# Kernel tuning notes

Measured on AMD Instinct MI355X. Metric: run time of the kernel, lower is better.

## Reference

```python
import jax, jax.numpy as jnp
import numpy as np

B, C, H, W = 8, 256, 64, 64
CI = 128  # inter_channels
EPS = 1e-5

def conv1x1(x, w, b):
    # x:[B,C,H,W], w:[O,C], b:[O] -> [B,O,H,W]
    return jnp.einsum('bchw,oc->bohw', x, w) + b[None, :, None, None]

def maxpool2(t):
    b, c, h, w = t.shape
    return t.reshape(b, c, h // 2, 2, w // 2, 2).max(axis=(3, 5))

def setup_inputs() -> dict:
    key = jax.random.key(0)
    ks = jax.random.split(key, 11)
    s_in = 1.0 / np.sqrt(C)
    s_ci = 1.0 / np.sqrt(CI)
    return {
        'x':        jax.random.normal(ks[0], (B, C, H, W), jnp.float32),
        'g_w':      jax.random.normal(ks[1], (CI, C), jnp.float32) * s_in,
        'g_b':      jax.random.normal(ks[2], (CI,), jnp.float32) * s_in,
        'theta_w':  jax.random.normal(ks[3], (CI, C), jnp.float32) * s_in,
        'theta_b':  jax.random.normal(ks[4], (CI,), jnp.float32) * s_in,
        'phi_w':    jax.random.normal(ks[5], (CI, C), jnp.float32) * s_in,
        'phi_b':    jax.random.normal(ks[6], (CI,), jnp.float32) * s_in,
        'w_w':      jax.random.normal(ks[7], (C, CI), jnp.float32) * s_ci,
        'w_b':      jax.random.normal(ks[8], (C,), jnp.float32) * s_ci,
        'bn_gamma': jax.random.normal(ks[9], (C,), jnp.float32) * 0.1 + 1.0,
        'bn_beta':  jax.random.normal(ks[10], (C,), jnp.float32) * 0.1,
    }

def reference(x, g_w, g_b, theta_w, theta_b, phi_w, phi_b, w_w, w_b, bn_gamma, bn_beta):
    b, c, h, w = x.shape
    n = h * w
    # g and phi are sub-sampled with 2x2 max pool -> Ns = n // 4
    g_x = maxpool2(conv1x1(x, g_w, g_b)).reshape(b, CI, -1)      # [B,CI,Ns]
    g_x = g_x.transpose(0, 2, 1)                                  # [B,Ns,CI]
    theta_x = conv1x1(x, theta_w, theta_b).reshape(b, CI, n)
    theta_x = theta_x.transpose(0, 2, 1)                          # [B,N,CI]
    phi_x = maxpool2(conv1x1(x, phi_w, phi_b)).reshape(b, CI, -1)  # [B,CI,Ns]
    f = jnp.einsum('bnc,bcm->bnm', theta_x, phi_x)                # [B,N,Ns] (no 1/sqrt(d) scale, faithful)
    f_div_c = jax.nn.softmax(f, axis=-1)
    y = jnp.einsum('bnm,bmc->bnc', f_div_c, g_x)                  # [B,N,CI]
    y = y.transpose(0, 2, 1).reshape(b, CI, h, w)
    wy = conv1x1(y, w_w, w_b)                                     # [B,C,H,W]
    # BatchNorm2d in training mode: batch stats over (B,H,W)
    mean = wy.mean(axis=(0, 2, 3), keepdims=True)
    var = wy.var(axis=(0, 2, 3), keepdims=True)
    wy_bn = (wy - mean) * jax.lax.rsqrt(var + EPS)
    wy_bn = wy_bn * bn_gamma[None, :, None, None] + bn_beta[None, :, None, None]
    return wy_bn + x
```

## Files before the change

kernel.cpp:

```cpp
#include <hip/hip_runtime.h>
#include <hip/hip_bf16.h>
#include <hip/hip_fp16.h>
#include <math.h>

#define B 8
#define C 256
#define HH 64
#define WW 64
#define NN 4096
#define CI 128
#define NS 1024
#define EPS 1e-5f

typedef __attribute__((ext_vector_type(8))) _Float16 f16x8;
typedef __attribute__((ext_vector_type(4))) float f32x4;

static __device__ __forceinline__ unsigned short f2h_bits(float f) {
    return __half_as_ushort(__float2half(f));
}

__global__ __launch_bounds__(256) void k_prep(const float* __restrict__ tw,
        const float* __restrict__ pw, const float* __restrict__ gw,
        const float* __restrict__ ww, unsigned short* __restrict__ wh) {
    int idx = blockIdx.x * 256 + threadIdx.x;
    int sel = idx >> 15, off = idx & 32767;
    const float* src = (sel == 0) ? tw : (sel == 1) ? pw : (sel == 2) ? gw : ww;
    wh[idx] = f2h_bits(src[off]);
}

__global__ __launch_bounds__(256) void k_xt(const float* __restrict__ x,
                                            unsigned short* __restrict__ xh) {
    __shared__ float s_t[64 * 65];
    int n0 = blockIdx.x * 64;
    int c0 = blockIdx.y * 64;
    int b  = blockIdx.z;
    int tid = threadIdx.x;
    #pragma unroll
    for (int k = 0; k < 16; ++k) {
        int idx = tid + k * 256;
        int cl = idx >> 6, nl = idx & 63;
        s_t[cl * 65 + nl] = x[((size_t)b * C + c0 + cl) * NN + n0 + nl];
    }
    __syncthreads();
    #pragma unroll
    for (int k = 0; k < 8; ++k) {
        int idx = tid + k * 256;
        int nl = idx >> 5, cp = (idx & 31) * 2;
        ushort2 o;
        o.x = f2h_bits(s_t[cp * 65 + nl]);
        o.y = f2h_bits(s_t[(cp + 1) * 65 + nl]);
        *(ushort2*)&xh[((size_t)b * NN + n0 + nl) * C + c0 + cp] = o;
    }
}

__global__ __launch_bounds__(256) void k_conv_theta(const unsigned short* __restrict__ xh,
        const unsigned short* __restrict__ twh, const float* __restrict__ tb,
        unsigned short* __restrict__ theta) {
    int blk = blockIdx.x;
    int tid = threadIdx.x;
    int lane = tid & 63, wv = tid >> 6;
    int lr = lane & 15, lh = lane >> 4;
    int rowf = blk * 64 + wv * 16 + lr;

    f32x4 acc[8];
    #pragma unroll
    for (int i = 0; i < 8; ++i) acc[i] = (f32x4){0.f, 0.f, 0.f, 0.f};

    const unsigned short* ap = xh + (size_t)rowf * C + lh * 8;
    #pragma unroll
    for (int kc = 0; kc < 8; ++kc) {
        f16x8 a = *(const f16x8*)(ap + kc * 32);
        #pragma unroll
        for (int ct = 0; ct < 8; ++ct) {
            f16x8 bf = *(const f16x8*)&twh[(ct * 16 + lr) * C + kc * 32 + lh * 8];
            acc[ct] = __builtin_amdgcn_mfma_f32_16x16x32_f16(a, bf, acc[ct], 0, 0, 0);
        }
    }
    int rowo = blk * 64 + wv * 16 + lh * 4;
    #pragma unroll
    for (int ct = 0; ct < 8; ++ct) {
        int ci = ct * 16 + lr;
        float bias = tb[ci];
        #pragma unroll
        for (int r = 0; r < 4; ++r)
            theta[(size_t)(rowo + r) * CI + ci] = f2h_bits(acc[ct][r] + bias);
    }
}

__global__ __launch_bounds__(512) void k_conv_pool2(const unsigned short* __restrict__ xh,
        const unsigned short* __restrict__ pwh, const unsigned short* __restrict__ gwh,
        const float* __restrict__ pb, const float* __restrict__ gb_,
        unsigned short* __restrict__ phi, unsigned short* __restrict__ gout) {
    int blk = blockIdx.x;
    int b   = blk >> 5;
    int mh  = blk & 31;
    int tid = threadIdx.x;
    int lane = tid & 63, wv = tid >> 6;
    int lr = lane & 15, lh = lane >> 4;
    int wn = wv & 3, wc = wv >> 2;
    size_t row0 = (size_t)blk * 128;

    f32x4 aP0[4], aP1[4], aG0[4], aG1[4];
    #pragma unroll
    for (int i = 0; i < 4; ++i) {
        aP0[i] = (f32x4){0,0,0,0}; aP1[i] = (f32x4){0,0,0,0};
        aG0[i] = (f32x4){0,0,0,0}; aG1[i] = (f32x4){0,0,0,0};
    }

    const unsigned short* ap0 = xh + (row0 + wn * 16 + lr) * C + lh * 8;
    const unsigned short* ap1 = ap0 + (size_t)64 * C;
    #pragma unroll
    for (int kc = 0; kc < 8; ++kc) {
        f16x8 a0 = *(const f16x8*)(ap0 + kc * 32);
        f16x8 a1 = *(const f16x8*)(ap1 + kc * 32);
        #pragma unroll
        for (int ct = 0; ct < 4; ++ct) {
            int wrow = (wc * 64 + ct * 16 + lr) * C + kc * 32 + lh * 8;
            f16x8 bp = *(const f16x8*)&pwh[wrow];
            f16x8 bg = *(const f16x8*)&gwh[wrow];
            aP0[ct] = __builtin_amdgcn_mfma_f32_16x16x32_f16(a0, bp, aP0[ct], 0, 0, 0);
            aP1[ct] = __builtin_amdgcn_mfma_f32_16x16x32_f16(a1, bp, aP1[ct], 0, 0, 0);
            aG0[ct] = __builtin_amdgcn_mfma_f32_16x16x32_f16(a0, bg, aG0[ct], 0, 0, 0);
            aG1[ct] = __builtin_amdgcn_mfma_f32_16x16x32_f16(a1, bg, aG1[ct], 0, 0, 0);
        }
    }
    #pragma unroll
    for (int ct = 0; ct < 4; ++ct) {
        int ci = wc * 64 + ct * 16 + lr;
        float biasP = pb[ci], biasG = gb_[ci];
        #pragma unroll
        for (int j = 0; j < 2; ++j) {
            int m = mh * 32 + wn * 8 + lh * 2 + j;
            float vP = fmaxf(fmaxf(aP0[ct][2*j], aP0[ct][2*j+1]),
                             fmaxf(aP1[ct][2*j], aP1[ct][2*j+1])) + biasP;
            float vG = fmaxf(fmaxf(aG0[ct][2*j], aG0[ct][2*j+1]),
                             fmaxf(aG1[ct][2*j], aG1[ct][2*j+1])) + biasG;
            phi[((size_t)b * NS + m) * CI + ci]  = f2h_bits(vP);
            gout[((size_t)b * CI + ci) * NS + m] = f2h_bits(vG);
        }
    }
}

#define SPH 136
#define SG  72
#define SP  72
__global__ __launch_bounds__(256) void k_attn_mfma(const unsigned short* __restrict__ theta,
        const unsigned short* __restrict__ phi, const unsigned short* __restrict__ g,
        unsigned short* __restrict__ y) {
    __shared__ unsigned short s_ph[64 * SPH];
    __shared__ unsigned short s_g[128 * SG];
    __shared__ unsigned short s_p[64 * SP];
    int rb = blockIdx.x;
    int b  = blockIdx.y;
    int tid = threadIdx.x;
    int lane = tid & 63, wv = tid >> 6;
    int lr = lane & 15, lh = lane >> 4;
    int row0 = rb * 64;
    int wrow = wv * 16;

    f16x8 a_th[4];
    {
        const unsigned short* tp = theta + ((size_t)b * NN + row0 + wrow + lr) * CI + lh * 8;
        #pragma unroll
        for (int kc = 0; kc < 4; ++kc) a_th[kc] = *(const f16x8*)(tp + kc * 32);
    }

    f32x4 yacc[8];
    #pragma unroll
    for (int i = 0; i < 8; ++i) yacc[i] = (f32x4){0.f, 0.f, 0.f, 0.f};
    float mrun[4] = {-1e30f, -1e30f, -1e30f, -1e30f};
    float lrun[4] = {0.f, 0.f, 0.f, 0.f};

    for (int mt = 0; mt < 16; ++mt) {
        __syncthreads();
        {
            const ushort4* src = (const ushort4*)(phi + ((size_t)b * NS + mt * 64) * CI);
            #pragma unroll
            for (int k = 0; k < 8; ++k) {
                int t = tid + k * 256;
                int r = t >> 5, cq = t & 31;
                ushort4 vv = src[r * 32 + cq];
                *(ushort4*)&s_ph[r * SPH + cq * 4] = vv;
            }
            const ushort4* sg = (const ushort4*)(g + (size_t)b * CI * NS);
            #pragma unroll
            for (int k = 0; k < 8; ++k) {
                int t = tid + k * 256;
                int ci = t >> 4, cq = t & 15;
                ushort4 vv = sg[ci * 256 + mt * 16 + cq];
                *(ushort4*)&s_g[ci * SG + cq * 4] = vv;
            }
        }
        __syncthreads();

        f32x4 S[4];
        #pragma unroll
        for (int nt = 0; nt < 4; ++nt) S[nt] = (f32x4){0.f, 0.f, 0.f, 0.f};
        #pragma unroll
        for (int nt = 0; nt < 4; ++nt) {
            #pragma unroll
            for (int kc = 0; kc < 4; ++kc) {
                f16x8 bf = *(const f16x8*)&s_ph[(nt * 16 + lr) * SPH + kc * 32 + lh * 8];
                S[nt] = __builtin_amdgcn_mfma_f32_16x16x32_f16(a_th[kc], bf, S[nt], 0, 0, 0);
            }
        }

        float rmax[4], rs[4], scale[4];
        #pragma unroll
        for (int r = 0; r < 4; ++r)
            rmax[r] = fmaxf(fmaxf(S[0][r], S[1][r]), fmaxf(S[2][r], S[3][r]));
        #pragma unroll
        for (int s = 1; s < 16; s <<= 1) {
            #pragma unroll
            for (int r = 0; r < 4; ++r) rmax[r] = fmaxf(rmax[r], __shfl_xor(rmax[r], s));
        }
        #pragma unroll
        for (int r = 0; r < 4; ++r) {
            float mnew = fmaxf(mrun[r], rmax[r]);
            scale[r] = __expf(mrun[r] - mnew);
            mrun[r] = mnew;
            rs[r] = 0.f;
        }
        #pragma unroll
        for (int nt = 0; nt < 4; ++nt) {
            #pragma unroll
            for (int r = 0; r < 4; ++r) {
                float e = __expf(S[nt][r] - mrun[r]);
                S[nt][r] = e;
                rs[r] += e;
            }
        }
        #pragma unroll
        for (int s = 1; s < 16; s <<= 1) {
            #pragma unroll
            for (int r = 0; r < 4; ++r) rs[r] += __shfl_xor(rs[r], s);
        }
        #pragma unroll
        for (int r = 0; r < 4; ++r) lrun[r] = lrun[r] * scale[r] + rs[r];
        #pragma unroll
        for (int i = 0; i < 8; ++i) {
            #pragma unroll
            for (int r = 0; r < 4; ++r) yacc[i][r] *= scale[r];
        }
        #pragma unroll
        for (int nt = 0; nt < 4; ++nt) {
            #pragma unroll
            for (int r = 0; r < 4; ++r)
                s_p[(wrow + lh * 4 + r) * SP + nt * 16 + lr] = f2h_bits(S[nt][r]);
        }

        f16x8 a_p[2];
        #pragma unroll
        for (int kc = 0; kc < 2; ++kc)
            a_p[kc] = *(const f16x8*)&s_p[(wrow + lr) * SP + kc * 32 + lh * 8];
        #pragma unroll
        for (int ct = 0; ct < 8; ++ct) {
            #pragma unroll
            for (int kc = 0; kc < 2; ++kc) {
                f16x8 bg = *(const f16x8*)&s_g[(ct * 16 + lr) * SG + kc * 32 + lh * 8];
                yacc[ct] = __builtin_amdgcn_mfma_f32_16x16x32_f16(a_p[kc], bg, yacc[ct], 0, 0, 0);
            }
        }
    }

    float inv[4];
    #pragma unroll
    for (int r = 0; r < 4; ++r) inv[r] = 1.f / lrun[r];
    #pragma unroll
    for (int ct = 0; ct < 8; ++ct) {
        #pragma unroll
        for (int r = 0; r < 4; ++r)
            y[((size_t)b * NN + row0 + wrow + lh * 4 + r) * CI + ct * 16 + lr] =
                f2h_bits(yacc[ct][r] * inv[r]);
    }
}

__global__ __launch_bounds__(256) void k_wconv(const unsigned short* __restrict__ y,
        const unsigned short* __restrict__ wwh, const float* __restrict__ wb,
        float* __restrict__ wy) {
    int blk = blockIdx.x;
    int b   = blk >> 6;
    int nloc = (blk & 63) * 64;
    int tid = threadIdx.x;
    int lane = tid & 63, wv = tid >> 6;
    int lr = lane & 15, lh = lane >> 4;

    f32x4 acc[4][4];
    #pragma unroll
    for (int i = 0; i < 4; ++i)
        #pragma unroll
        for (int j = 0; j < 4; ++j) acc[i][j] = (f32x4){0.f, 0.f, 0.f, 0.f};

    const unsigned short* yb = y + ((size_t)b * NN + nloc) * CI;
    #pragma unroll
    for (int kc = 0; kc < 4; ++kc) {
        f16x8 a[4], bf[4];
        #pragma unroll
        for (int at = 0; at < 4; ++at)
            a[at] = *(const f16x8*)&wwh[(wv * 64 + at * 16 + lr) * CI + kc * 32 + lh * 8];
        #pragma unroll
        for (int bt = 0; bt < 4; ++bt)
            bf[bt] = *(const f16x8*)&yb[(size_t)(bt * 16 + lr) * CI + kc * 32 + lh * 8];
        #pragma unroll
        for (int at = 0; at < 4; ++at)
            #pragma unroll
            for (int bt = 0; bt < 4; ++bt)
                acc[at][bt] = __builtin_amdgcn_mfma_f32_16x16x32_f16(a[at], bf[bt], acc[at][bt], 0, 0, 0);
    }
    #pragma unroll
    for (int at = 0; at < 4; ++at) {
        #pragma unroll
        for (int r = 0; r < 4; ++r) {
            int co = wv * 64 + at * 16 + lh * 4 + r;
            float bias = wb[co];
            float* wp = wy + ((size_t)b * C + co) * NN + nloc;
            #pragma unroll
            for (int bt = 0; bt < 4; ++bt)
                wp[bt * 16 + lr] = acc[at][bt][r] + bias;
        }
    }
}

__global__ __launch_bounds__(256) void k_stats(const float* __restrict__ wy,
                                               float* __restrict__ stats) {
    int c = blockIdx.x;
    int tid = threadIdx.x;
    float s = 0.f, sq = 0.f;
    for (int b = 0; b < B; ++b) {
        const float* p = wy + ((size_t)b * C + c) * NN;
        #pragma unroll 4
        for (int k = 0; k < 16; ++k) {
            float v = p[tid + k * 256];
            s += v;
            sq = fmaf(v, v, sq);
        }
    }
    #pragma unroll
    for (int o = 32; o >= 1; o >>= 1) {
        s  += __shfl_down(s, o);
        sq += __shfl_down(sq, o);
    }
    __shared__ float rs[4], rq[4];
    int lane = tid & 63, wv = tid >> 6;
    if (lane == 0) { rs[wv] = s; rq[wv] = sq; }
    __syncthreads();
    if (tid == 0) {
        stats[c]       = rs[0] + rs[1] + rs[2] + rs[3];
        stats[256 + c] = rq[0] + rq[1] + rq[2] + rq[3];
    }
}

__global__ __launch_bounds__(256) void k_bn_out(const float* __restrict__ wy,
        const float* __restrict__ x, const float* __restrict__ stats,
        const float* __restrict__ gamma, const float* __restrict__ beta,
        float* __restrict__ out) {
    size_t idx = (size_t)blockIdx.x * 256 + threadIdx.x;
    int c = (int)(((idx * 4) >> 12) & 255);
    float mean = stats[c] * (1.f / 32768.f);
    float var  = stats[256 + c] * (1.f / 32768.f) - mean * mean;
    float sc = gamma[c] * rsqrtf(var + EPS);
    float sh = beta[c] - mean * sc;
    float4 w4 = ((const float4*)wy)[idx];
    float4 x4 = ((const float4*)x)[idx];
    float4 o;
    o.x = fmaf(w4.x, sc, sh) + x4.x;
    o.y = fmaf(w4.y, sc, sh) + x4.y;
    o.z = fmaf(w4.z, sc, sh) + x4.z;
    o.w = fmaf(w4.w, sc, sh) + x4.w;
    ((float4*)out)[idx] = o;
}

extern "C" void kernel_launch(void* const* d_in, const int* in_sizes, int n_in,
                              void* d_out, int out_size, void* d_ws, size_t ws_size,
                              hipStream_t stream) {
    const float* x    = (const float*)d_in[0];
    const float* g_w  = (const float*)d_in[1];
    const float* g_b  = (const float*)d_in[2];
    const float* th_w = (const float*)d_in[3];
    const float* th_b = (const float*)d_in[4];
    const float* ph_w = (const float*)d_in[5];
    const float* ph_b = (const float*)d_in[6];
    const float* w_w  = (const float*)d_in[7];
    const float* w_b  = (const float*)d_in[8];
    const float* bn_g = (const float*)d_in[9];
    const float* bn_b = (const float*)d_in[10];
    float* out = (float*)d_out;

    char* w0 = (char*)d_ws;
    float*          wy    = (float*)w0;
    unsigned short* xh    = (unsigned short*)w0;
    unsigned short* theta = (unsigned short*)(w0 + 16777216);
    unsigned short* wh    = (unsigned short*)(w0 + 33554432);
    unsigned short* twh   = wh;
    unsigned short* pwh   = wh + 32768;
    unsigned short* gwh   = wh + 65536;
    unsigned short* wwh   = wh + 98304;
    unsigned short* phi   = (unsigned short*)(w0 + 33816576);
    unsigned short* gx    = (unsigned short*)(w0 + 35913728);
    unsigned short* yh    = (unsigned short*)(w0 + 38010880);
    float*          stats = (float*)(w0 + 46399488);

    k_prep<<<512, 256, 0, stream>>>(th_w, ph_w, g_w, w_w, wh);
    k_xt<<<dim3(64, 4, B), 256, 0, stream>>>(x, xh);
    k_conv_theta<<<512, 256, 0, stream>>>(xh, twh, th_b, theta);
    k_conv_pool2<<<256, 512, 0, stream>>>(xh, pwh, gwh, ph_b, g_b, phi, gx);
    k_attn_mfma<<<dim3(64, B), 256, 0, stream>>>(theta, phi, gx, yh);
    k_wconv<<<512, 256, 0, stream>>>(yh, wwh, w_b, wy);
    k_stats<<<256, 256, 0, stream>>>(wy, stats);
    k_bn_out<<<8192, 256, 0, stream>>>(wy, x, stats, bn_g, bn_b, out);
}
```

Before: 150.2 us.

## Fuse conv kernels, double-buffer attention tiles, store wy in fp16 with fused stats

Weight conversion is folded into the transpose kernel, and the theta conv is merged into the phi/g pooling conv so each x tile is read once. The attention loop now prefetches the next phi/g tile into registers and double-buffers shared memory, using setprio around MFMA blocks. The w-conv writes wy as fp16 and emits per-block partial sums, which replaces the full-tensor stats pass with a small reduction and halves traffic in the BN kernel. Storing wy in fp16 loses precision before the batch norm.

```diff
diff --git a/kernel.cpp b/kernel.cpp
--- a/kernel.cpp
+++ b/kernel.cpp
@@ -18,23 +18,32 @@
 static __device__ __forceinline__ unsigned short f2h_bits(float f) {
     return __half_as_ushort(__float2half(f));
 }
-
-__global__ __launch_bounds__(256) void k_prep(const float* __restrict__ tw,
-        const float* __restrict__ pw, const float* __restrict__ gw,
-        const float* __restrict__ ww, unsigned short* __restrict__ wh) {
-    int idx = blockIdx.x * 256 + threadIdx.x;
-    int sel = idx >> 15, off = idx & 32767;
-    const float* src = (sel == 0) ? tw : (sel == 1) ? pw : (sel == 2) ? gw : ww;
-    wh[idx] = f2h_bits(src[off]);
+static __device__ __forceinline__ float h2f(unsigned short u) {
+    return __half2float(__ushort_as_half(u));
 }
 
 __global__ __launch_bounds__(256) void k_xt(const float* __restrict__ x,
-                                            unsigned short* __restrict__ xh) {
+        unsigned short* __restrict__ xh,
+        const float* __restrict__ tw, const float* __restrict__ pw,
+        const float* __restrict__ gw, const float* __restrict__ ww,
+        unsigned short* __restrict__ wh) {
+    int tid = threadIdx.x;
+    if (blockIdx.x == 64) {
+        int inst = blockIdx.y * B + blockIdx.z;
+        int base = inst * 4096;
+        #pragma unroll
+        for (int k = 0; k < 16; ++k) {
+            int idx = base + tid + k * 256;
+            int sel = idx >> 15, off = idx & 32767;
+            const float* src = (sel == 0) ? tw : (sel == 1) ? pw : (sel == 2) ? gw : ww;
+            wh[idx] = f2h_bits(src[off]);
+        }
+        return;
+    }
     __shared__ float s_t[64 * 65];
     int n0 = blockIdx.x * 64;
     int c0 = blockIdx.y * 64;
     int b  = blockIdx.z;
-    int tid = threadIdx.x;
     #pragma unroll
     for (int k = 0; k < 16; ++k) {
         int idx = tid + k * 256;
@@ -53,44 +62,12 @@
     }
 }
 
-__global__ __launch_bounds__(256) void k_conv_theta(const unsigned short* __restrict__ xh,
-        const unsigned short* __restrict__ twh, const float* __restrict__ tb,
-        unsigned short* __restrict__ theta) {
-    int blk = blockIdx.x;
-    int tid = threadIdx.x;
-    int lane = tid & 63, wv = tid >> 6;
-    int lr = lane & 15, lh = lane >> 4;
-    int rowf = blk * 64 + wv * 16 + lr;
-
-    f32x4 acc[8];
-    #pragma unroll
-    for (int i = 0; i < 8; ++i) acc[i] = (f32x4){0.f, 0.f, 0.f, 0.f};
-
-    const unsigned short* ap = xh + (size_t)rowf * C + lh * 8;
-    #pragma unroll
-    for (int kc = 0; kc < 8; ++kc) {
-        f16x8 a = *(const f16x8*)(ap + kc * 32);
-        #pragma unroll
-        for (int ct = 0; ct < 8; ++ct) {
-            f16x8 bf = *(const f16x8*)&twh[(ct * 16 + lr) * C + kc * 32 + lh * 8];
-            acc[ct] = __builtin_amdgcn_mfma_f32_16x16x32_f16(a, bf, acc[ct], 0, 0, 0);
-        }
-    }
-    int rowo = blk * 64 + wv * 16 + lh * 4;
-    #pragma unroll
-    for (int ct = 0; ct < 8; ++ct) {
-        int ci = ct * 16 + lr;
-        float bias = tb[ci];
-        #pragma unroll
-        for (int r = 0; r < 4; ++r)
-            theta[(size_t)(rowo + r) * CI + ci] = f2h_bits(acc[ct][r] + bias);
-    }
-}
-
-__global__ __launch_bounds__(512) void k_conv_pool2(const unsigned short* __restrict__ xh,
-        const unsigned short* __restrict__ pwh, const unsigned short* __restrict__ gwh,
-        const float* __restrict__ pb, const float* __restrict__ gb_,
-        unsigned short* __restrict__ phi, unsigned short* __restrict__ gout) {
+__global__ __launch_bounds__(512) void k_convs(const unsigned short* __restrict__ xh,
+        const unsigned short* __restrict__ twh, const unsigned short* __restrict__ pwh,
+        const unsigned short* __restrict__ gwh,
+        const float* __restrict__ tb, const float* __restrict__ pb, const float* __restrict__ gb_,
+        unsigned short* __restrict__ theta, unsigned short* __restrict__ phi,
+        unsigned short* __restrict__ gout) {
     int blk = blockIdx.x;
     int b   = blk >> 5;
     int mh  = blk & 31;
@@ -100,7 +77,10 @@
     int wn = wv & 3, wc = wv >> 2;
     size_t row0 = (size_t)blk * 128;
 
+    f32x4 accT[8];
     f32x4 aP0[4], aP1[4], aG0[4], aG1[4];
+    #pragma unroll
+    for (int i = 0; i < 8; ++i) accT[i] = (f32x4){0,0,0,0};
     #pragma unroll
     for (int i = 0; i < 4; ++i) {
         aP0[i] = (f32x4){0,0,0,0}; aP1[i] = (f32x4){0,0,0,0};
@@ -113,6 +93,12 @@
     for (int kc = 0; kc < 8; ++kc) {
         f16x8 a0 = *(const f16x8*)(ap0 + kc * 32);
         f16x8 a1 = *(const f16x8*)(ap1 + kc * 32);
+        f16x8 aT = (wv < 4) ? a0 : a1;
+        #pragma unroll
+        for (int ct = 0; ct < 8; ++ct) {
+            f16x8 bt_ = *(const f16x8*)&twh[(ct * 16 + lr) * C + kc * 32 + lh * 8];
+            accT[ct] = __builtin_amdgcn_mfma_f32_16x16x32_f16(aT, bt_, accT[ct], 0, 0, 0);
+        }
         #pragma unroll
         for (int ct = 0; ct < 4; ++ct) {
             int wrow = (wc * 64 + ct * 16 + lr) * C + kc * 32 + lh * 8;
@@ -125,6 +111,14 @@
         }
     }
     #pragma unroll
+    for (int ct = 0; ct < 8; ++ct) {
+        int ci = ct * 16 + lr;
+        float bias = tb[ci];
+        #pragma unroll
+        for (int r = 0; r < 4; ++r)
+            theta[(row0 + wv * 16 + lh * 4 + r) * CI + ci] = f2h_bits(accT[ct][r] + bias);
+    }
+    #pragma unroll
     for (int ct = 0; ct < 4; ++ct) {
         int ci = wc * 64 + ct * 16 + lr;
         float biasP = pb[ci], biasG = gb_[ci];
@@ -143,12 +137,12 @@
 
 #define SPH 136
 #define SG  72
-#define SP  72
+#define SP  68
 __global__ __launch_bounds__(256) void k_attn_mfma(const unsigned short* __restrict__ theta,
         const unsigned short* __restrict__ phi, const unsigned short* __restrict__ g,
         unsigned short* __restrict__ y) {
-    __shared__ unsigned short s_ph[64 * SPH];
-    __shared__ unsigned short s_g[128 * SG];
+    __shared__ unsigned short s_ph[2][64 * SPH];
+    __shared__ unsigned short s_g[2][128 * SG];
     __shared__ unsigned short s_p[64 * SP];
     int rb = blockIdx.x;
     int b  = blockIdx.y;
@@ -165,45 +159,56 @@
         for (int kc = 0; kc < 4; ++kc) a_th[kc] = *(const f16x8*)(tp + kc * 32);
     }
 
+    const ushort4* phsrc = (const ushort4*)(phi + (size_t)b * NS * CI);
+    const ushort4* gsrc  = (const ushort4*)(g + (size_t)b * CI * NS);
+
     f32x4 yacc[8];
     #pragma unroll
     for (int i = 0; i < 8; ++i) yacc[i] = (f32x4){0.f, 0.f, 0.f, 0.f};
     float mrun[4] = {-1e30f, -1e30f, -1e30f, -1e30f};
     float lrun[4] = {0.f, 0.f, 0.f, 0.f};
 
+    ushort4 rph[8], rg[8];
+    #pragma unroll
+    for (int k = 0; k < 8; ++k) {
+        int t = tid + k * 256;
+        rph[k] = phsrc[(t >> 5) * 32 + (t & 31)];
+        rg[k]  = gsrc[(t >> 4) * 256 + (t & 15)];
+    }
+    #pragma unroll
+    for (int k = 0; k < 8; ++k) {
+        int t = tid + k * 256;
+        *(ushort4*)&s_ph[0][(t >> 5) * SPH + (t & 31) * 4] = rph[k];
+        *(ushort4*)&s_g[0][(t >> 4) * SG + (t & 15) * 4]   = rg[k];
+    }
+    __syncthreads();
+    int cur = 0;
+
     for (int mt = 0; mt < 16; ++mt) {
-        __syncthreads();
-        {
-            const ushort4* src = (const ushort4*)(phi + ((size_t)b * NS + mt * 64) * CI);
+        if (mt < 15) {
             #pragma unroll
             for (int k = 0; k < 8; ++k) {
                 int t = tid + k * 256;
-                int r = t >> 5, cq = t & 31;
-                ushort4 vv = src[r * 32 + cq];
-                *(ushort4*)&s_ph[r * SPH + cq * 4] = vv;
-            }
-            const ushort4* sg = (const ushort4*)(g + (size_t)b * CI * NS);
-            #pragma unroll
-            for (int k = 0; k < 8; ++k) {
-                int t = tid + k * 256;
-                int ci = t >> 4, cq = t & 15;
-                ushort4 vv = sg[ci * 256 + mt * 16 + cq];
-                *(ushort4*)&s_g[ci * SG + cq * 4] = vv;
-            }
-        }
-        __syncthreads();
+                rph[k] = phsrc[((mt + 1) * 64 + (t >> 5)) * 32 + (t & 31)];
+                rg[k]  = gsrc[(t >> 4) * 256 + (mt + 1) * 16 + (t & 15)];
+            }
+        }
+        const unsigned short* ph = s_ph[cur];
+        const unsigned short* sg_ = s_g[cur];
 
         f32x4 S[4];
         #pragma unroll
         for (int nt = 0; nt < 4; ++nt) S[nt] = (f32x4){0.f, 0.f, 0.f, 0.f};
+        __builtin_amdgcn_s_setprio(1);
         #pragma unroll
         for (int nt = 0; nt < 4; ++nt) {
             #pragma unroll
             for (int kc = 0; kc < 4; ++kc) {
-                f16x8 bf = *(const f16x8*)&s_ph[(nt * 16 + lr) * SPH + kc * 32 + lh * 8];
+                f16x8 bf = *(const f16x8*)&ph[(nt * 16 + lr) * SPH + kc * 32 + lh * 8];
                 S[nt] = __builtin_amdgcn_mfma_f32_16x16x32_f16(a_th[kc], bf, S[nt], 0, 0, 0);
             }
         }
+        __builtin_amdgcn_s_setprio(0);
 
         float rmax[4], rs[4], scale[4];
         #pragma unroll
@@ -253,13 +258,27 @@
         #pragma unroll
         for (int kc = 0; kc < 2; ++kc)
             a_p[kc] = *(const f16x8*)&s_p[(wrow + lr) * SP + kc * 32 + lh * 8];
+        __builtin_amdgcn_s_setprio(1);
         #pragma unroll
         for (int ct = 0; ct < 8; ++ct) {
             #pragma unroll
             for (int kc = 0; kc < 2; ++kc) {
-                f16x8 bg = *(const f16x8*)&s_g[(ct * 16 + lr) * SG + kc * 32 + lh * 8];
+                f16x8 bg = *(const f16x8*)&sg_[(ct * 16 + lr) * SG + kc * 32 + lh * 8];
                 yacc[ct] = __builtin_amdgcn_mfma_f32_16x16x32_f16(a_p[kc], bg, yacc[ct], 0, 0, 0);
             }
+        }
+        __builtin_amdgcn_s_setprio(0);
+
+        if (mt < 15) {
+            int nxt = cur ^ 1;
+            #pragma unroll
+            for (int k = 0; k < 8; ++k) {
+                int t = tid + k * 256;
+                *(ushort4*)&s_ph[nxt][(t >> 5) * SPH + (t & 31) * 4] = rph[k];
+                *(ushort4*)&s_g[nxt][(t >> 4) * SG + (t & 15) * 4]   = rg[k];
+            }
+            __syncthreads();
+            cur = nxt;
         }
     }
 
@@ -277,7 +296,7 @@
 
 __global__ __launch_bounds__(256) void k_wconv(const unsigned short* __restrict__ y,
         const unsigned short* __restrict__ wwh, const float* __restrict__ wb,
-        float* __restrict__ wy) {
+        unsigned short* __restrict__ wyh, float* __restrict__ psum, float* __restrict__ psq) {
     int blk = blockIdx.x;
     int b   = blk >> 6;
     int nloc = (blk & 63) * 64;
@@ -313,61 +332,72 @@
         for (int r = 0; r < 4; ++r) {
             int co = wv * 64 + at * 16 + lh * 4 + r;
             float bias = wb[co];
-            float* wp = wy + ((size_t)b * C + co) * NN + nloc;
-            #pragma unroll
-            for (int bt = 0; bt < 4; ++bt)
-                wp[bt * 16 + lr] = acc[at][bt][r] + bias;
-        }
-    }
-}
-
-__global__ __launch_bounds__(256) void k_stats(const float* __restrict__ wy,
-                                               float* __restrict__ stats) {
+            unsigned short* wp = wyh + ((size_t)b * C + co) * NN + nloc;
+            float s = 0.f, q = 0.f;
+            #pragma unroll
+            for (int bt = 0; bt < 4; ++bt) {
+                float v = acc[at][bt][r] + bias;
+                wp[bt * 16 + lr] = f2h_bits(v);
+                s += v;
+                q = fmaf(v, v, q);
+            }
+            #pragma unroll
+            for (int o = 1; o < 16; o <<= 1) {
+                s += __shfl_xor(s, o);
+                q += __shfl_xor(q, o);
+            }
+            if (lr == 0) {
+                psum[co * 512 + blk] = s;
+                psq[co * 512 + blk]  = q;
+            }
+        }
+    }
+}
+
+__global__ __launch_bounds__(64) void k_stats_r(const float* __restrict__ psum,
+        const float* __restrict__ psq, float* __restrict__ stats) {
     int c = blockIdx.x;
-    int tid = threadIdx.x;
-    float s = 0.f, sq = 0.f;
-    for (int b = 0; b < B; ++b) {
-        const float* p = wy + ((size_t)b * C + c) * NN;
-        #pragma unroll 4
-        for (int k = 0; k < 16; ++k) {
-            float v = p[tid + k * 256];
-            s += v;
-            sq = fmaf(v, v, sq);
-        }
+    int lane = threadIdx.x;
+    float s = 0.f, q = 0.f;
+    #pragma unroll
+    for (int k = 0; k < 8; ++k) {
+        s += psum[c * 512 + lane + k * 64];
+        q += psq[c * 512 + lane + k * 64];
     }
     #pragma unroll
     for (int o = 32; o >= 1; o >>= 1) {
-        s  += __shfl_down(s, o);
-        sq += __shfl_down(sq, o);
-    }
-    __shared__ float rs[4], rq[4];
-    int lane = tid & 63, wv = tid >> 6;
-    if (lane == 0) { rs[wv] = s; rq[wv] = sq; }
-    __syncthreads();
-    if (tid == 0) {
-        stats[c]       = rs[0] + rs[1] + rs[2] + rs[3];
-        stats[256 + c] = rq[0] + rq[1] + rq[2] + rq[3];
-    }
-}
-
-__global__ __launch_bounds__(256) void k_bn_out(const float* __restrict__ wy,
+        s += __shfl_down(s, o);
+        q += __shfl_down(q, o);
+    }
+    if (lane == 0) { stats[c] = s; stats[256 + c] = q; }
+}
+
+__global__ __launch_bounds__(256) void k_bn_out(const unsigned short* __restrict__ wyh,
         const float* __restrict__ x, const float* __restrict__ stats,
         const float* __restrict__ gamma, const float* __restrict__ beta,
         float* __restrict__ out) {
-    size_t idx = (size_t)blockIdx.x * 256 + threadIdx.x;
-    int c = (int)(((idx * 4) >> 12) & 255);
+    size_t t = (size_t)blockIdx.x * 256 + threadIdx.x;
+    size_t base = t * 8;
+    int c = (int)((base >> 12) & 255);
     float mean = stats[c] * (1.f / 32768.f);
     float var  = stats[256 + c] * (1.f / 32768.f) - mean * mean;
     float sc = gamma[c] * rsqrtf(var + EPS);
     float sh = beta[c] - mean * sc;
-    float4 w4 = ((const float4*)wy)[idx];
-    float4 x4 = ((const float4*)x)[idx];
-    float4 o;
-    o.x = fmaf(w4.x, sc, sh) + x4.x;
-    o.y = fmaf(w4.y, sc, sh) + x4.y;
-    o.z = fmaf(w4.z, sc, sh) + x4.z;
-    o.w = fmaf(w4.w, sc, sh) + x4.w;
-    ((float4*)out)[idx] = o;
+    ushort4 w0 = *(const ushort4*)&wyh[base];
+    ushort4 w1 = *(const ushort4*)&wyh[base + 4];
+    float4 x0 = *(const float4*)&x[base];
+    float4 x1 = *(const float4*)&x[base + 4];
+    float4 o0, o1;
+    o0.x = fmaf(h2f(w0.x), sc, sh) + x0.x;
+    o0.y = fmaf(h2f(w0.y), sc, sh) + x0.y;
+    o0.z = fmaf(h2f(w0.z), sc, sh) + x0.z;
+    o0.w = fmaf(h2f(w0.w), sc, sh) + x0.w;
+    o1.x = fmaf(h2f(w1.x), sc, sh) + x1.x;
+    o1.y = fmaf(h2f(w1.y), sc, sh) + x1.y;
+    o1.z = fmaf(h2f(w1.z), sc, sh) + x1.z;
+    o1.w = fmaf(h2f(w1.w), sc, sh) + x1.w;
+    *(float4*)&out[base]     = o0;
+    *(float4*)&out[base + 4] = o1;
 }
 
 extern "C" void kernel_launch(void* const* d_in, const int* in_sizes, int n_in,
@@ -387,25 +417,25 @@
     float* out = (float*)d_out;
 
     char* w0 = (char*)d_ws;
-    float*          wy    = (float*)w0;
     unsigned short* xh    = (unsigned short*)w0;
     unsigned short* theta = (unsigned short*)(w0 + 16777216);
-    unsigned short* wh    = (unsigned short*)(w0 + 33554432);
+    unsigned short* wh    = (unsigned short*)(w0 + 25165824);
     unsigned short* twh   = wh;
     unsigned short* pwh   = wh + 32768;
     unsigned short* gwh   = wh + 65536;
     unsigned short* wwh   = wh + 98304;
-    unsigned short* phi   = (unsigned short*)(w0 + 33816576);
-    unsigned short* gx    = (unsigned short*)(w0 + 35913728);
-    unsigned short* yh    = (unsigned short*)(w0 + 38010880);
-    float*          stats = (float*)(w0 + 46399488);
-
-    k_prep<<<512, 256, 0, stream>>>(th_w, ph_w, g_w, w_w, wh);
-    k_xt<<<dim3(64, 4, B), 256, 0, stream>>>(x, xh);
-    k_conv_theta<<<512, 256, 0, stream>>>(xh, twh, th_b, theta);
-    k_conv_pool2<<<256, 512, 0, stream>>>(xh, pwh, gwh, ph_b, g_b, phi, gx);
+    unsigned short* phi   = (unsigned short*)(w0 + 25427968);
+    unsigned short* gx    = (unsigned short*)(w0 + 27525120);
+    unsigned short* yh    = (unsigned short*)(w0 + 29622272);
+    unsigned short* wyh   = (unsigned short*)(w0 + 38010880);
+    float*          psum  = (float*)(w0 + 54788096);
+    float*          psq   = (float*)(w0 + 55312384);
+    float*          stats = (float*)(w0 + 55836672);
+
+    k_xt<<<dim3(65, 4, B), 256, 0, stream>>>(x, xh, th_w, ph_w, g_w, w_w, wh);
+    k_convs<<<256, 512, 0, stream>>>(xh, twh, pwh, gwh, th_b, ph_b, g_b, theta, phi, gx);
     k_attn_mfma<<<dim3(64, B), 256, 0, stream>>>(theta, phi, gx, yh);
-    k_wconv<<<512, 256, 0, stream>>>(yh, wwh, w_b, wy);
-    k_stats<<<256, 256, 0, stream>>>(wy, stats);
-    k_bn_out<<<8192, 256, 0, stream>>>(wy, x, stats, bn_g, bn_b, out);
-}
+    k_wconv<<<512, 256, 0, stream>>>(yh, wwh, w_b, wyh, psum, psq);
+    k_stats_r<<<256, 64, 0, stream>>>(psum, psq, stats);
+    k_bn_out<<<4096, 256, 0, stream>>>(wyh, x, stats, bn_g, bn_b, out);
+}
```

New measurement: 131.8 us. 12.2% less time.
